# Kernel tuning notes

Hardware: AMD Instinct MI355X
Metric: run time of the kernel (lower is better)

Reference implementation:

```python
import jax, jax.numpy as jnp
import numpy as np

SEQ, B, H2 = 4096, 64, 256  # seq_len, batch, 2*hidden_size


def setup_inputs() -> dict:
    key = jax.random.key(0)
    k0, k1, k2, k3 = jax.random.split(key, 4)
    uni = lambda k, shape: jax.random.uniform(k, shape, jnp.float32, -0.1, 0.1)
    return {
        "encoder_outputs": jax.random.normal(k0, (SEQ, B, H2), jnp.float32),
        "weight_W_word": uni(k1, (H2, H2)),
        "bias_word": uni(k2, (H2, 1)),
        "weight_proj_word": uni(k3, (H2, 1)),
    }


def reference(encoder_outputs, weight_W_word, bias_word, weight_proj_word):
    # tanh(x @ W + b): [seq, batch, 2H]
    squish = jnp.tanh(
        jnp.einsum("sbd,de->sbe", encoder_outputs, weight_W_word)
        + bias_word[:, 0]
    )
    # projection to scalar score per (seq, batch): [seq, batch]
    attn = jnp.einsum("sbe,e->sb", squish, weight_proj_word[:, 0])
    # softmax over seq dim (original: softmax on [batch, seq] over dim 1)
    attn_norm = jax.nn.softmax(attn.T, axis=1)  # [batch, seq]
    # weighted sum over seq: [1, batch, 2H]
    vectors = jnp.einsum("sb,sbd->bd", attn_norm.T, encoder_outputs)[None]
    return (vectors, attn_norm)
```

## Files before the change

kernel.cpp:

```cpp
#include <hip/hip_runtime.h>
#include <hip/hip_bf16.h>

#define SEQ 4096
#define NB 64
#define H2 256
#define MROWS (SEQ * NB)

typedef short bf16x8 __attribute__((ext_vector_type(8)));
typedef int   i32x4  __attribute__((ext_vector_type(4)));
typedef float f32x4  __attribute__((ext_vector_type(4)));

__device__ __forceinline__ float fast_tanh(float x) {
    float e = __expf(2.0f * x);
    return 1.0f - 2.0f * __builtin_amdgcn_rcpf(e + 1.0f);
}

__global__ __launch_bounds__(256)
void pack_w_kernel(const float* __restrict__ W, __hip_bfloat16* __restrict__ Wp) {
    int t = blockIdx.x * 256 + threadIdx.x;
    int l  = t & 63;
    int n  = (t >> 6) & 15;
    int kk = t >> 10;
    int e  = n * 16 + (l & 15);
    int d0 = kk * 32 + 8 * (l >> 4);
    union { __hip_bfloat16 h[8]; i32x4 v; } cv;
#pragma unroll
    for (int i = 0; i < 8; ++i) cv.h[i] = __float2bfloat16(W[(d0 + i) * H2 + e]);
    *reinterpret_cast<i32x4*>(&Wp[(size_t)t * 8]) = cv.v;
}

__global__ __launch_bounds__(256, 2)
void mfma_logits_kernel(const float* __restrict__ enc,
                        const __hip_bfloat16* __restrict__ Wp,
                        const float* __restrict__ bias,
                        const float* __restrict__ proj,
                        float* __restrict__ attnS) {
    __shared__ __hip_bfloat16 aT[2][128][40];
    __shared__ __hip_bfloat16 wT[2][8192];

    const int tid  = threadIdx.x;
    const int lane = tid & 63;
    const int w    = tid >> 6;
    const long r0  = (long)blockIdx.x * 128;

    f32x4 acc[2][16];
#pragma unroll
    for (int rt = 0; rt < 2; ++rt)
#pragma unroll
        for (int n = 0; n < 16; ++n) acc[rt][n] = (f32x4)(0.0f);

#pragma unroll
    for (int it = 0; it < 4; ++it) {
        int q = it * 256 + tid;
        int row = q >> 3;
        int dc = (q & 7) * 4;
        float4 v = *reinterpret_cast<const float4*>(&enc[(r0 + row) * H2 + dc]);
        union { __hip_bfloat16 h[4]; uint2 u; } cv;
        cv.h[0] = __float2bfloat16(v.x); cv.h[1] = __float2bfloat16(v.y);
        cv.h[2] = __float2bfloat16(v.z); cv.h[3] = __float2bfloat16(v.w);
        *reinterpret_cast<uint2*>(&aT[0][row][dc]) = cv.u;
        i32x4 wv = *reinterpret_cast<const i32x4*>(&Wp[q * 8]);
        *reinterpret_cast<i32x4*>(&wT[0][q * 8]) = wv;
    }
    __syncthreads();

    int buf = 0;
#pragma unroll
    for (int kk = 0; kk < 8; ++kk) {
        float4 av[4]; i32x4 wv[4];
        if (kk < 7) {
#pragma unroll
            for (int it = 0; it < 4; ++it) {
                int q = it * 256 + tid;
                int row = q >> 3;
                int dc = (q & 7) * 4;
                av[it] = *reinterpret_cast<const float4*>(
                    &enc[(r0 + row) * H2 + (kk + 1) * 32 + dc]);
                wv[it] = *reinterpret_cast<const i32x4*>(&Wp[(kk + 1) * 8192 + q * 8]);
            }
        }
        bf16x8 af[2];
#pragma unroll
        for (int rt = 0; rt < 2; ++rt)
            af[rt] = *reinterpret_cast<const bf16x8*>(
                &aT[buf][w * 32 + rt * 16 + (lane & 15)][8 * (lane >> 4)]);
#pragma unroll
        for (int n = 0; n < 16; ++n) {
            bf16x8 bv = *reinterpret_cast<const bf16x8*>(&wT[buf][(n * 64 + lane) * 8]);
            acc[0][n] = __builtin_amdgcn_mfma_f32_16x16x32_bf16(af[0], bv, acc[0][n], 0, 0, 0);
            acc[1][n] = __builtin_amdgcn_mfma_f32_16x16x32_bf16(af[1], bv, acc[1][n], 0, 0, 0);
        }
        if (kk < 7) {
#pragma unroll
            for (int it = 0; it < 4; ++it) {
                int q = it * 256 + tid;
                int row = q >> 3;
                int dc = (q & 7) * 4;
                union { __hip_bfloat16 h[4]; uint2 u; } cv;
                cv.h[0] = __float2bfloat16(av[it].x); cv.h[1] = __float2bfloat16(av[it].y);
                cv.h[2] = __float2bfloat16(av[it].z); cv.h[3] = __float2bfloat16(av[it].w);
                *reinterpret_cast<uint2*>(&aT[buf ^ 1][row][dc]) = cv.u;
                *reinterpret_cast<i32x4*>(&wT[buf ^ 1][q * 8]) = wv[it];
            }
        }
        __syncthreads();
        buf ^= 1;
    }

    float biasv[16], projv[16];
#pragma unroll
    for (int n = 0; n < 16; ++n) {
        int e = n * 16 + (lane & 15);
        biasv[n] = bias[e];
        projv[n] = proj[e];
    }
#pragma unroll
    for (int rt = 0; rt < 2; ++rt) {
        float pv[4];
#pragma unroll
        for (int r = 0; r < 4; ++r) {
            float p = 0.0f;
#pragma unroll
            for (int n = 0; n < 16; ++n) {
                float z = acc[rt][n][r] + biasv[n];
                p += projv[n] * fast_tanh(z);
            }
            p += __shfl_xor(p, 1);
            p += __shfl_xor(p, 2);
            p += __shfl_xor(p, 4);
            p += __shfl_xor(p, 8);
            pv[r] = p;
        }
        if ((lane & 15) == 0) {
            long row = r0 + w * 32 + rt * 16 + (lane >> 4) * 4;
            float4 o; o.x = pv[0]; o.y = pv[1]; o.z = pv[2]; o.w = pv[3];
            *reinterpret_cast<float4*>(&attnS[row]) = o;
        }
    }
}

__global__ void r17_softmax(const float* __restrict__ attnS,
                            float* __restrict__ out_attn) {
    __shared__ float sL[SEQ];
    __shared__ float red[256];
    const int b = blockIdx.x;
    const int t = threadIdx.x;

    float lm = -1e30f;
    for (int s = t; s < SEQ; s += 256) {
        float v = attnS[(size_t)s * NB + b];
        sL[s] = v;
        lm = fmaxf(lm, v);
    }
    red[t] = lm;
    __syncthreads();
    for (int h = 128; h > 0; h >>= 1) {
        if (t < h) red[t] = fmaxf(red[t], red[t + h]);
        __syncthreads();
    }
    const float gmax = red[0];
    __syncthreads();

    float ls = 0.0f;
    for (int s = t; s < SEQ; s += 256) {
        float e = __expf(sL[s] - gmax);
        sL[s] = e;
        ls += e;
    }
    red[t] = ls;
    __syncthreads();
    for (int h = 128; h > 0; h >>= 1) {
        if (t < h) red[t] += red[t + h];
        __syncthreads();
    }
    const float inv = 1.0f / red[0];

    for (int s = t; s < SEQ; s += 256) {
        out_attn[(size_t)b * SEQ + s] = sL[s] * inv;
    }
}

__global__ void r17_wsum(const float* __restrict__ enc,
                         const float* __restrict__ out_attn,
                         float* __restrict__ partials) {
    __shared__ float wl[256];
    const int b = blockIdx.x & 63;
    const int c = blockIdx.x >> 6;
    const int t = threadIdx.x;
    wl[t] = out_attn[(size_t)b * SEQ + c * 256 + t];
    __syncthreads();
    float acc = 0.0f;
    for (int si = 0; si < 256; ++si) {
        acc = fmaf(wl[si],
                   enc[((size_t)(c * 256 + si) * NB + b) * H2 + t],
                   acc);
    }
    partials[((size_t)c * NB + b) * H2 + t] = acc;
}

__global__ void r17_reduce(const float* __restrict__ partials,
                           float* __restrict__ out_vec) {
    const int b = blockIdx.x;
    const int t = threadIdx.x;
    float a = 0.0f;
    for (int c = 0; c < 16; ++c)
        a += partials[((size_t)c * NB + b) * H2 + t];
    out_vec[(size_t)b * H2 + t] = a;
}

extern "C" void kernel_launch(void* const* d_in, const int* in_sizes, int n_in,
                              void* d_out, int out_size, void* d_ws, size_t ws_size,
                              hipStream_t stream) {
    const float* enc  = (const float*)d_in[0];
    const float* W    = (const float*)d_in[1];
    const float* bias = (const float*)d_in[2];
    const float* proj = (const float*)d_in[3];

    float* out      = (float*)d_out;
    float* out_vec  = out;
    float* out_attn = out + NB * H2;

    char* ws = (char*)d_ws;
    __hip_bfloat16* Wp = (__hip_bfloat16*)ws;
    float* attnS    = (float*)(ws + 131072);
    float* partials = (float*)(ws + 131072 + (1u << 20));

    hipLaunchKernelGGL(pack_w_kernel,     dim3(32),          dim3(256), 0, stream,
                       W, Wp);
    hipLaunchKernelGGL(mfma_logits_kernel, dim3(MROWS / 128), dim3(256), 0, stream,
                       enc, Wp, bias, proj, attnS);
    hipLaunchKernelGGL(r17_softmax,       dim3(NB),          dim3(256), 0, stream,
                       attnS, out_attn);
    hipLaunchKernelGGL(r17_wsum,          dim3(16 * NB),     dim3(256), 0, stream,
                       enc, out_attn, partials);
    hipLaunchKernelGGL(r17_reduce,        dim3(NB),          dim3(256), 0, stream,
                       partials, out_vec);
}
```

Before: 130.9 us.

## Drop LDS staging in logits GEMM and vectorize weighted-sum kernel

The logits kernel no longer stages encoder and weight tiles through double-buffered shared memory with barriers. Each wave now loads its A fragment directly from global memory and reads the packed W fragments straight from global/L2. It uses 64-row blocks with higher occupancy but gives up operand reuse across rows. The weighted-sum kernel switches to float4 loads with four sequence slices per block, combined through shared memory, which shortens the serial dependency chain.

```diff
diff --git a/kernel.cpp b/kernel.cpp
--- a/kernel.cpp
+++ b/kernel.cpp
@@ -29,117 +29,72 @@
     *reinterpret_cast<i32x4*>(&Wp[(size_t)t * 8]) = cv.v;
 }
 
-__global__ __launch_bounds__(256, 2)
+__global__ __launch_bounds__(256, 4)
 void mfma_logits_kernel(const float* __restrict__ enc,
                         const __hip_bfloat16* __restrict__ Wp,
                         const float* __restrict__ bias,
                         const float* __restrict__ proj,
                         float* __restrict__ attnS) {
-    __shared__ __hip_bfloat16 aT[2][128][40];
-    __shared__ __hip_bfloat16 wT[2][8192];
-
-    const int tid  = threadIdx.x;
-    const int lane = tid & 63;
-    const int w    = tid >> 6;
-    const long r0  = (long)blockIdx.x * 128;
-
-    f32x4 acc[2][16];
-#pragma unroll
-    for (int rt = 0; rt < 2; ++rt)
-#pragma unroll
-        for (int n = 0; n < 16; ++n) acc[rt][n] = (f32x4)(0.0f);
-
-#pragma unroll
-    for (int it = 0; it < 4; ++it) {
-        int q = it * 256 + tid;
-        int row = q >> 3;
-        int dc = (q & 7) * 4;
-        float4 v = *reinterpret_cast<const float4*>(&enc[(r0 + row) * H2 + dc]);
-        union { __hip_bfloat16 h[4]; uint2 u; } cv;
-        cv.h[0] = __float2bfloat16(v.x); cv.h[1] = __float2bfloat16(v.y);
-        cv.h[2] = __float2bfloat16(v.z); cv.h[3] = __float2bfloat16(v.w);
-        *reinterpret_cast<uint2*>(&aT[0][row][dc]) = cv.u;
-        i32x4 wv = *reinterpret_cast<const i32x4*>(&Wp[q * 8]);
-        *reinterpret_cast<i32x4*>(&wT[0][q * 8]) = wv;
-    }
-    __syncthreads();
-
-    int buf = 0;
+    const int tid   = threadIdx.x;
+    const int lane  = tid & 63;
+    const int w     = tid >> 6;
+    const int rloc  = lane & 15;
+    const int kslot = lane >> 4;
+    const long r0   = (long)blockIdx.x * 64;
+    const long row  = r0 + w * 16 + rloc;
+
+    const float* encRow = enc + (size_t)row * H2 + kslot * 8;
+    const __hip_bfloat16* WpL = Wp + (size_t)lane * 8;
+
+    f32x4 acc[16];
+#pragma unroll
+    for (int n = 0; n < 16; ++n) acc[n] = (f32x4)(0.0f);
+
 #pragma unroll
     for (int kk = 0; kk < 8; ++kk) {
-        float4 av[4]; i32x4 wv[4];
-        if (kk < 7) {
-#pragma unroll
-            for (int it = 0; it < 4; ++it) {
-                int q = it * 256 + tid;
-                int row = q >> 3;
-                int dc = (q & 7) * 4;
-                av[it] = *reinterpret_cast<const float4*>(
-                    &enc[(r0 + row) * H2 + (kk + 1) * 32 + dc]);
-                wv[it] = *reinterpret_cast<const i32x4*>(&Wp[(kk + 1) * 8192 + q * 8]);
-            }
+        float4 a0 = *reinterpret_cast<const float4*>(encRow + kk * 32);
+        float4 a1 = *reinterpret_cast<const float4*>(encRow + kk * 32 + 4);
+        union { __hip_bfloat16 h[8]; bf16x8 v; } af;
+        af.h[0] = __float2bfloat16(a0.x); af.h[1] = __float2bfloat16(a0.y);
+        af.h[2] = __float2bfloat16(a0.z); af.h[3] = __float2bfloat16(a0.w);
+        af.h[4] = __float2bfloat16(a1.x); af.h[5] = __float2bfloat16(a1.y);
+        af.h[6] = __float2bfloat16(a1.z); af.h[7] = __float2bfloat16(a1.w);
+#pragma unroll
+        for (int n = 0; n < 16; ++n) {
+            bf16x8 bv = *reinterpret_cast<const bf16x8*>(WpL + (size_t)(kk * 16 + n) * 512);
+            acc[n] = __builtin_amdgcn_mfma_f32_16x16x32_bf16(af.v, bv, acc[n], 0, 0, 0);
         }
-        bf16x8 af[2];
-#pragma unroll
-        for (int rt = 0; rt < 2; ++rt)
-            af[rt] = *reinterpret_cast<const bf16x8*>(
-                &aT[buf][w * 32 + rt * 16 + (lane & 15)][8 * (lane >> 4)]);
-#pragma unroll
-        for (int n = 0; n < 16; ++n) {
-            bf16x8 bv = *reinterpret_cast<const bf16x8*>(&wT[buf][(n * 64 + lane) * 8]);
-            acc[0][n] = __builtin_amdgcn_mfma_f32_16x16x32_bf16(af[0], bv, acc[0][n], 0, 0, 0);
-            acc[1][n] = __builtin_amdgcn_mfma_f32_16x16x32_bf16(af[1], bv, acc[1][n], 0, 0, 0);
-        }
-        if (kk < 7) {
-#pragma unroll
-            for (int it = 0; it < 4; ++it) {
-                int q = it * 256 + tid;
-                int row = q >> 3;
-                int dc = (q & 7) * 4;
-                union { __hip_bfloat16 h[4]; uint2 u; } cv;
-                cv.h[0] = __float2bfloat16(av[it].x); cv.h[1] = __float2bfloat16(av[it].y);
-                cv.h[2] = __float2bfloat16(av[it].z); cv.h[3] = __float2bfloat16(av[it].w);
-                *reinterpret_cast<uint2*>(&aT[buf ^ 1][row][dc]) = cv.u;
-                *reinterpret_cast<i32x4*>(&wT[buf ^ 1][q * 8]) = wv[it];
-            }
-        }
-        __syncthreads();
-        buf ^= 1;
     }
 
     float biasv[16], projv[16];
 #pragma unroll
     for (int n = 0; n < 16; ++n) {
-        int e = n * 16 + (lane & 15);
+        int e = n * 16 + rloc;
         biasv[n] = bias[e];
         projv[n] = proj[e];
     }
-#pragma unroll
-    for (int rt = 0; rt < 2; ++rt) {
-        float pv[4];
-#pragma unroll
-        for (int r = 0; r < 4; ++r) {
-            float p = 0.0f;
-#pragma unroll
-            for (int n = 0; n < 16; ++n) {
-                float z = acc[rt][n][r] + biasv[n];
-                p += projv[n] * fast_tanh(z);
-            }
-            p += __shfl_xor(p, 1);
-            p += __shfl_xor(p, 2);
-            p += __shfl_xor(p, 4);
-            p += __shfl_xor(p, 8);
-            pv[r] = p;
+    float pv[4];
+#pragma unroll
+    for (int r = 0; r < 4; ++r) {
+        float p = 0.0f;
+#pragma unroll
+        for (int n = 0; n < 16; ++n) {
+            p += projv[n] * fast_tanh(acc[n][r] + biasv[n]);
         }
-        if ((lane & 15) == 0) {
-            long row = r0 + w * 32 + rt * 16 + (lane >> 4) * 4;
-            float4 o; o.x = pv[0]; o.y = pv[1]; o.z = pv[2]; o.w = pv[3];
-            *reinterpret_cast<float4*>(&attnS[row]) = o;
-        }
-    }
-}
-
-__global__ void r17_softmax(const float* __restrict__ attnS,
+        p += __shfl_xor(p, 1);
+        p += __shfl_xor(p, 2);
+        p += __shfl_xor(p, 4);
+        p += __shfl_xor(p, 8);
+        pv[r] = p;
+    }
+    if (rloc == 0) {
+        long orow = r0 + w * 16 + kslot * 4;
+        float4 o; o.x = pv[0]; o.y = pv[1]; o.z = pv[2]; o.w = pv[3];
+        *reinterpret_cast<float4*>(&attnS[orow]) = o;
+    }
+}
+
+__global__ void r18_softmax(const float* __restrict__ attnS,
                             float* __restrict__ out_attn) {
     __shared__ float sL[SEQ];
     __shared__ float red[256];
@@ -180,25 +135,46 @@
     }
 }
 
-__global__ void r17_wsum(const float* __restrict__ enc,
-                         const float* __restrict__ out_attn,
-                         float* __restrict__ partials) {
+__global__ __launch_bounds__(256)
+void r18_wsum(const float* __restrict__ enc,
+              const float* __restrict__ out_attn,
+              float* __restrict__ partials) {
     __shared__ float wl[256];
-    const int b = blockIdx.x & 63;
-    const int c = blockIdx.x >> 6;
-    const int t = threadIdx.x;
+    __shared__ float4 pf[4][64];
+    const int b  = blockIdx.x & 63;
+    const int c  = blockIdx.x >> 6;
+    const int t  = threadIdx.x;
+    const int dq = t & 63;
+    const int sq = t >> 6;
+
     wl[t] = out_attn[(size_t)b * SEQ + c * 256 + t];
     __syncthreads();
-    float acc = 0.0f;
-    for (int si = 0; si < 256; ++si) {
-        acc = fmaf(wl[si],
-                   enc[((size_t)(c * 256 + si) * NB + b) * H2 + t],
-                   acc);
-    }
-    partials[((size_t)c * NB + b) * H2 + t] = acc;
-}
-
-__global__ void r17_reduce(const float* __restrict__ partials,
+
+    float4 acc = make_float4(0.f, 0.f, 0.f, 0.f);
+    const size_t base = ((size_t)(c * 256 + sq * 64) * NB + b) * H2 + dq * 4;
+#pragma unroll 4
+    for (int j = 0; j < 64; ++j) {
+        float wv = wl[sq * 64 + j];
+        float4 ev = *reinterpret_cast<const float4*>(&enc[base + (size_t)j * NB * H2]);
+        acc.x = fmaf(wv, ev.x, acc.x);
+        acc.y = fmaf(wv, ev.y, acc.y);
+        acc.z = fmaf(wv, ev.z, acc.z);
+        acc.w = fmaf(wv, ev.w, acc.w);
+    }
+    pf[sq][dq] = acc;
+    __syncthreads();
+    if (sq == 0) {
+        float4 a = pf[0][dq], b1 = pf[1][dq], c1 = pf[2][dq], d1 = pf[3][dq];
+        float4 o;
+        o.x = a.x + b1.x + c1.x + d1.x;
+        o.y = a.y + b1.y + c1.y + d1.y;
+        o.z = a.z + b1.z + c1.z + d1.z;
+        o.w = a.w + b1.w + c1.w + d1.w;
+        *reinterpret_cast<float4*>(&partials[((size_t)c * NB + b) * H2 + dq * 4]) = o;
+    }
+}
+
+__global__ void r18_reduce(const float* __restrict__ partials,
                            float* __restrict__ out_vec) {
     const int b = blockIdx.x;
     const int t = threadIdx.x;
@@ -225,14 +201,14 @@
     float* attnS    = (float*)(ws + 131072);
     float* partials = (float*)(ws + 131072 + (1u << 20));
 
-    hipLaunchKernelGGL(pack_w_kernel,     dim3(32),          dim3(256), 0, stream,
+    hipLaunchKernelGGL(pack_w_kernel,      dim3(32),         dim3(256), 0, stream,
                        W, Wp);
-    hipLaunchKernelGGL(mfma_logits_kernel, dim3(MROWS / 128), dim3(256), 0, stream,
+    hipLaunchKernelGGL(mfma_logits_kernel, dim3(MROWS / 64), dim3(256), 0, stream,
                        enc, Wp, bias, proj, attnS);
-    hipLaunchKernelGGL(r17_softmax,       dim3(NB),          dim3(256), 0, stream,
+    hipLaunchKernelGGL(r18_softmax,        dim3(NB),         dim3(256), 0, stream,
                        attnS, out_attn);
-    hipLaunchKernelGGL(r17_wsum,          dim3(16 * NB),     dim3(256), 0, stream,
+    hipLaunchKernelGGL(r18_wsum,           dim3(16 * NB),    dim3(256), 0, stream,
                        enc, out_attn, partials);
-    hipLaunchKernelGGL(r17_reduce,        dim3(NB),          dim3(256), 0, stream,
+    hipLaunchKernelGGL(r18_reduce,         dim3(NB),         dim3(256), 0, stream,
                        partials, out_vec);
 }
```

New measurement: 175.8 us. 34.3% more time.
